# Optimization experiments

Measured on AMD Instinct MI355X. Metric: run time of the kernel, lower is better.

## Reference

```python
import jax, jax.numpy as jnp
import numpy as np

N_HEAD = 16
D_MODEL = 1024
D_K = D_MODEL // N_HEAD  # 64, also d_v
B, S = 8, 1024


def setup_inputs() -> dict:
    key = jax.random.key(0)
    ks = jax.random.split(key, 7)
    sc = 1.0 / np.sqrt(D_MODEL)
    return {
        "q": jax.random.normal(ks[0], (B, S, D_MODEL), jnp.float32),
        "k": jax.random.normal(ks[1], (B, S, D_MODEL), jnp.float32),
        "v": jax.random.normal(ks[2], (B, S, D_MODEL), jnp.float32),
        "Wq": jax.random.normal(ks[3], (N_HEAD, D_MODEL, D_K), jnp.float32) * sc,
        "Wk": jax.random.normal(ks[4], (N_HEAD, D_MODEL, D_K), jnp.float32) * sc,
        "Wv": jax.random.normal(ks[5], (D_MODEL, D_K), jnp.float32) * sc,  # shared across heads
        "Wo": jax.random.normal(ks[6], (D_K, D_MODEL), jnp.float32) * (1.0 / np.sqrt(D_K)),
    }


def reference(q, k, v, Wq, Wk, Wv, Wo):
    # Faithful to original: qs, ks, vs are ALL projected from q (k, v args unused),
    # and Wv is shared across all heads. Dropout is identity (rate 0 / eval).
    qs = jnp.einsum('bsd,hdk->hbsk', q, Wq)          # [H,B,S,dk]
    kk = jnp.einsum('bsd,hdk->hbsk', q, Wk)          # [H,B,S,dk]
    vs = jnp.einsum('bsd,dk->bsk', q, Wv)            # [B,S,dv] shared
    scale = 1.0 / jnp.sqrt(jnp.asarray(D_K, jnp.float32))
    scores = jnp.einsum('hbik,hbjk->hbij', qs, kk) * scale  # [H,B,S,S]
    attn = jax.nn.softmax(scores, axis=-1)
    head = jnp.einsum('hbij,bjk->hbik', attn, vs)    # [H,B,S,dv]
    pooled = jnp.mean(head, axis=0)                  # mean over heads, not concat
    out = jnp.einsum('bsk,kd->bsd', pooled, Wo)      # [B,S,d_model]
    return (out, attn)
```

## Files before the change

kernel.cpp:

```cpp
#include <hip/hip_runtime.h>
#include <hip/hip_bf16.h>
#include <stdint.h>

#define NC 2112

typedef __attribute__((ext_vector_type(8))) short bf16x8;
typedef __attribute__((ext_vector_type(4))) float f32x4;

static __device__ __forceinline__ unsigned short f2bf(float f) {
  uint32_t u = __builtin_bit_cast(uint32_t, f);
  u += 0x7FFFu + ((u >> 16) & 1u);
  return (unsigned short)(u >> 16);
}
static __device__ __forceinline__ unsigned short f2bf_n(float f) {
  __hip_bfloat16 h = __float2bfloat16(f);
  return __builtin_bit_cast(unsigned short, h);
}
static __device__ __forceinline__ float bf2f(unsigned short u) {
  return __builtin_bit_cast(float, ((uint32_t)u) << 16);
}
static __device__ __forceinline__ void gload16(const unsigned short* g, unsigned short* l) {
  __builtin_amdgcn_global_load_lds((const __attribute__((address_space(1))) void*)g,
                                   (__attribute__((address_space(3))) void*)l, 16, 0, 0);
}

__global__ void k_convert_q(const float* __restrict__ q, unsigned short* __restrict__ qbf) {
  int i = blockIdx.x * blockDim.x + threadIdx.x;
  float4 v = ((const float4*)q)[i];
  ushort4 o;
  o.x = f2bf(v.x); o.y = f2bf(v.y); o.z = f2bf(v.z); o.w = f2bf(v.w);
  ((ushort4*)qbf)[i] = o;
}

__global__ void k_build_wcatT(const float* __restrict__ Wq, const float* __restrict__ Wk,
                              const float* __restrict__ Wv, unsigned short* __restrict__ wt) {
  int t = blockIdx.x * blockDim.x + threadIdx.x;
  int c = t >> 7;
  int k0 = (t & 127) << 3;
  unsigned short o[8];
#pragma unroll
  for (int i = 0; i < 8; ++i) {
    int k = k0 + i;
    float v;
    if (c < 1024)      v = Wq[((size_t)(c >> 6) * 1024 + k) * 64 + (c & 63)];
    else if (c < 2048) v = Wk[((size_t)((c - 1024) >> 6) * 1024 + k) * 64 + (c & 63)];
    else               v = Wv[(size_t)k * 64 + (c - 2048)];
    o[i] = f2bf(v);
  }
  *(ushort4*)&wt[(size_t)c * 1024 + k0]     = *(ushort4*)&o[0];
  *(ushort4*)&wt[(size_t)c * 1024 + k0 + 4] = *(ushort4*)&o[4];
}

__global__ __launch_bounds__(256) void k_gemm(const unsigned short* __restrict__ A,
                                              const unsigned short* __restrict__ Bt,
                                              unsigned short* __restrict__ C,
                                              unsigned short* __restrict__ vst) {
  __shared__ unsigned short As[128 * 32];
  __shared__ unsigned short Bs[128 * 32];
  const int L = blockIdx.x;
  const int wi = (L & 7) * 136 + (L >> 3);
  const int tn = wi % 17, tm = wi / 17;
  const int rowBase = tm * 128, colBase = tn * 128;
  const int t = threadIdx.x;
  const int wave = t >> 6, lane = t & 63;
  const int wm = wave >> 1, wn = wave & 1;
  const int l15 = lane & 15, l4 = lane >> 4;
  f32x4 acc[4][4] = {};
  for (int kt = 0; kt < 1024; kt += 32) {
#pragma unroll
    for (int i = 0; i < 2; ++i) {
      int e = (t + i * 256) * 8;
      int r = e >> 5, c = e & 31;
      gload16(&A[(size_t)(rowBase + r) * 1024 + kt + c], &As[e]);
      int rb = colBase + r; rb = rb < NC ? rb : (NC - 1);
      gload16(&Bt[(size_t)rb * 1024 + kt + c], &Bs[e]);
    }
    __syncthreads();
    bf16x8 af[4], bfr[4];
#pragma unroll
    for (int m = 0; m < 4; ++m) af[m] = *(const bf16x8*)&As[(wm * 64 + m * 16 + l15) * 32 + l4 * 8];
#pragma unroll
    for (int n = 0; n < 4; ++n) bfr[n] = *(const bf16x8*)&Bs[(wn * 64 + n * 16 + l15) * 32 + l4 * 8];
#pragma unroll
    for (int m = 0; m < 4; ++m)
#pragma unroll
      for (int n = 0; n < 4; ++n)
        acc[m][n] = __builtin_amdgcn_mfma_f32_16x16x32_bf16(af[m], bfr[n], acc[m][n], 0, 0, 0);
    __syncthreads();
  }
#pragma unroll
  for (int m = 0; m < 4; ++m)
#pragma unroll
    for (int n = 0; n < 4; ++n) {
      int col = colBase + wn * 64 + n * 16 + l15;
      int row0 = rowBase + wm * 64 + m * 16 + l4 * 4;
      if (col < 2048) {
#pragma unroll
        for (int i = 0; i < 4; ++i)
          C[(size_t)(row0 + i) * NC + col] = f2bf_n(acc[m][n][i]);
      } else if (col < NC) {
        int d = col - 2048;
#pragma unroll
        for (int i = 0; i < 4; ++i) {
          int rg = row0 + i;
          vst[((size_t)(rg >> 10) * 64 + d) * 1024 + (rg & 1023)] = f2bf_n(acc[m][n][i]);
        }
      }
    }
}

__global__ __launch_bounds__(256, 4) void k_attn(const unsigned short* __restrict__ G,
                                                 const unsigned short* __restrict__ vst,
                                                 float* __restrict__ attn,
                                                 float* __restrict__ head) {
  __shared__ unsigned short SP[16][1032];
  __shared__ float rs[16][4];
  const int L = blockIdx.x;
  const int wi = (L & 7) * 1024 + (L >> 3);
  const int qt = wi & 63, b = (wi >> 6) & 7, h = wi >> 9;
  const int t = threadIdx.x, wave = t >> 6, lane = t & 63;
  const int l15 = lane & 15, l4 = lane >> 4;

  const unsigned short* Gb = G + (size_t)b * 1024 * NC;

  bf16x8 qf[2];
#pragma unroll
  for (int ks = 0; ks < 2; ++ks)
    qf[ks] = *(const bf16x8*)&Gb[(size_t)(qt * 16 + l15) * NC + h * 64 + ks * 32 + l4 * 8];

  const float scale = 0.125f;
  float psum[4] = {};
#pragma unroll
  for (int quarter = 0; quarter < 4; ++quarter) {
    bf16x8 kf[4][2];
#pragma unroll
    for (int kt = 0; kt < 4; ++kt) {
      int k0 = wave * 256 + quarter * 64 + kt * 16;
#pragma unroll
      for (int ks = 0; ks < 2; ++ks)
        kf[kt][ks] = *(const bf16x8*)&Gb[(size_t)(k0 + l15) * NC + 1024 + h * 64 + ks * 32 + l4 * 8];
    }
#pragma unroll
    for (int kt = 0; kt < 4; ++kt) {
      int k0 = wave * 256 + quarter * 64 + kt * 16;
      f32x4 s0 = {};
      s0 = __builtin_amdgcn_mfma_f32_16x16x32_bf16(qf[0], kf[kt][0], s0, 0, 0, 0);
      s0 = __builtin_amdgcn_mfma_f32_16x16x32_bf16(qf[1], kf[kt][1], s0, 0, 0, 0);
#pragma unroll
      for (int i = 0; i < 4; ++i) {
        unsigned short u = f2bf_n(__expf(s0[i] * scale));
        SP[l4 * 4 + i][k0 + l15] = u;
        psum[i] += bf2f(u);
      }
    }
  }
#pragma unroll
  for (int off = 1; off < 16; off <<= 1)
#pragma unroll
    for (int i = 0; i < 4; ++i)
      psum[i] += __shfl_xor(psum[i], off);
  if (l15 == 0) {
#pragma unroll
    for (int i = 0; i < 4; ++i)
      rs[l4 * 4 + i][wave] = psum[i];
  }
  __syncthreads();

  float winv[4], pinv[4];
#pragma unroll
  for (int rr = 0; rr < 4; ++rr) {
    float4 a = *(const float4*)&rs[wave * 4 + rr][0];
    winv[rr] = 1.0f / (a.x + a.y + a.z + a.w);
  }
#pragma unroll
  for (int i = 0; i < 4; ++i) {
    float4 a = *(const float4*)&rs[l4 * 4 + i][0];
    pinv[i] = 1.0f / (a.x + a.y + a.z + a.w);
  }

  size_t attn_base = ((size_t)(h * 8 + b) * 1024 + (size_t)qt * 16) * 1024;
#pragma unroll
  for (int rr = 0; rr < 4; ++rr) {
    int row = wave * 4 + rr;
    float inv = winv[rr];
#pragma unroll
    for (int c = 0; c < 2; ++c) {
      uint4 u = *(const uint4*)&SP[row][c * 512 + lane * 8];
      f32x4 p0 = {bf2f((unsigned short)(u.x & 0xFFFF)) * inv,
                  bf2f((unsigned short)(u.x >> 16)) * inv,
                  bf2f((unsigned short)(u.y & 0xFFFF)) * inv,
                  bf2f((unsigned short)(u.y >> 16)) * inv};
      f32x4 p1 = {bf2f((unsigned short)(u.z & 0xFFFF)) * inv,
                  bf2f((unsigned short)(u.z >> 16)) * inv,
                  bf2f((unsigned short)(u.w & 0xFFFF)) * inv,
                  bf2f((unsigned short)(u.w >> 16)) * inv};
      float* ab = &attn[attn_base + (size_t)row * 1024 + c * 512 + lane * 8];
      __builtin_nontemporal_store(p0, (f32x4*)ab);
      __builtin_nontemporal_store(p1, (f32x4*)(ab + 4));
    }
  }

  const unsigned short* vb = vst + ((size_t)b * 64 + wave * 16 + l15) * 1024;
  const unsigned short* pr = &SP[l15][0];
  f32x4 o0 = {}, o1 = {};
#pragma unroll 8
  for (int jt = 0; jt < 32; jt += 2) {
    bf16x8 pa0 = *(const bf16x8*)&pr[jt * 32 + l4 * 8];
    bf16x8 bv0 = *(const bf16x8*)&vb[jt * 32 + l4 * 8];
    o0 = __builtin_amdgcn_mfma_f32_16x16x32_bf16(pa0, bv0, o0, 0, 0, 0);
    bf16x8 pa1 = *(const bf16x8*)&pr[(jt + 1) * 32 + l4 * 8];
    bf16x8 bv1 = *(const bf16x8*)&vb[(jt + 1) * 32 + l4 * 8];
    o1 = __builtin_amdgcn_mfma_f32_16x16x32_bf16(pa1, bv1, o1, 0, 0, 0);
  }
  float* hb = head + (((size_t)(h * 8 + b) * 1024) + qt * 16) * 64 + wave * 16;
#pragma unroll
  for (int i = 0; i < 4; ++i)
    hb[(size_t)(l4 * 4 + i) * 64 + l15] = (o0[i] + o1[i]) * pinv[i];
}

__global__ __launch_bounds__(256) void k_final(const float* __restrict__ head,
                                               const float* __restrict__ Wo,
                                               float* __restrict__ out) {
  __shared__ float Ps[16][68];
  __shared__ float Ws[64][132];
  const int rt = blockIdx.x;
  const int r0 = rt * 16;
  const int t = threadIdx.x;
  {
    int r = t >> 4, k4 = (t & 15) * 4;
    float4 acc = {0.f, 0.f, 0.f, 0.f};
#pragma unroll
    for (int hh = 0; hh < 16; ++hh) {
      float4 v = *(const float4*)&head[((size_t)hh * 8192 + r0 + r) * 64 + k4];
      acc.x += v.x; acc.y += v.y; acc.z += v.z; acc.w += v.w;
    }
    const float s = 1.0f / 16.0f;
    Ps[r][k4] = acc.x * s; Ps[r][k4 + 1] = acc.y * s;
    Ps[r][k4 + 2] = acc.z * s; Ps[r][k4 + 3] = acc.w * s;
  }
  const int ty = t >> 4, tx = t & 15;
  for (int dt = 0; dt < 8; ++dt) {
    int d0 = dt * 128;
#pragma unroll
    for (int j = 0; j < 8; ++j) {
      int e = t + j * 256;
      int k = e >> 5, c4 = (e & 31) * 4;
      *(float4*)&Ws[k][c4] = *(const float4*)&Wo[(size_t)k * 1024 + d0 + c4];
    }
    __syncthreads();
    float acc[8] = {};
    for (int k = 0; k < 64; ++k) {
      float a0 = Ps[ty][k];
      float4 b0 = *(const float4*)&Ws[k][tx * 8];
      float4 b1 = *(const float4*)&Ws[k][tx * 8 + 4];
      acc[0] += a0 * b0.x; acc[1] += a0 * b0.y; acc[2] += a0 * b0.z; acc[3] += a0 * b0.w;
      acc[4] += a0 * b1.x; acc[5] += a0 * b1.y; acc[6] += a0 * b1.z; acc[7] += a0 * b1.w;
    }
    float4 v0 = {acc[0], acc[1], acc[2], acc[3]};
    float4 v1 = {acc[4], acc[5], acc[6], acc[7]};
    size_t o = (size_t)(r0 + ty) * 1024 + d0 + tx * 8;
    *(float4*)&out[o]     = v0;
    *(float4*)&out[o + 4] = v1;
    __syncthreads();
  }
}

extern "C" void kernel_launch(void* const* d_in, const int* in_sizes, int n_in,
                              void* d_out, int out_size, void* d_ws, size_t ws_size,
                              hipStream_t stream) {
  const float* q  = (const float*)d_in[0];
  const float* Wq = (const float*)d_in[3];
  const float* Wk = (const float*)d_in[4];
  const float* Wv = (const float*)d_in[5];
  const float* Wo = (const float*)d_in[6];

  char* ws = (char*)d_ws;
  unsigned short* qbf   = (unsigned short*)(ws + 0);
  unsigned short* wcatT = (unsigned short*)(ws + 16777216);
  unsigned short* G     = (unsigned short*)(ws + 21102592);
  unsigned short* vst   = (unsigned short*)(ws + 55705600);
  float*          head  = (float*)(ws + 56754176);

  float* out  = (float*)d_out;
  float* attn = out + (size_t)8 * 1024 * 1024;

  hipLaunchKernelGGL(k_convert_q,   dim3(8192), dim3(256), 0, stream, q, qbf);
  hipLaunchKernelGGL(k_build_wcatT, dim3(1056), dim3(256), 0, stream, Wq, Wk, Wv, wcatT);
  hipLaunchKernelGGL(k_gemm,        dim3(1088), dim3(256), 0, stream, qbf, wcatT, G, vst);
  hipLaunchKernelGGL(k_attn,        dim3(8192), dim3(256), 0, stream, G, vst, attn, head);
  hipLaunchKernelGGL(k_final,       dim3(512),  dim3(256), 0, stream, head, Wo, out);
}
```

Baseline: 401.5 us.

## Restructure attention into two-pass per-wave softmax with recomputed scores

Each wave now owns 16 query rows and sweeps all 1024 keys itself. A first pass computes only the row sums of exp(scores). A second pass recomputes QK^T, writes normalized probabilities straight to attn, and accumulates P·V in 64-key chunks through a small per-wave LDS tile. This removes the 16x1024 LDS buffer, the block-wide barrier and the cross-wave sum exchange, and cuts the grid from 8192 to 2048 blocks. The cost is doubling the QK^T MFMA work and K reads, and attn is now written with scattered 4-byte nontemporal stores instead of 16-byte vector stores.

```diff
diff --git a/kernel.cpp b/kernel.cpp
--- a/kernel.cpp
+++ b/kernel.cpp
@@ -113,109 +113,95 @@
                                                  const unsigned short* __restrict__ vst,
                                                  float* __restrict__ attn,
                                                  float* __restrict__ head) {
-  __shared__ unsigned short SP[16][1032];
-  __shared__ float rs[16][4];
+  __shared__ unsigned short SP[4][16][72];
   const int L = blockIdx.x;
-  const int wi = (L & 7) * 1024 + (L >> 3);
-  const int qt = wi & 63, b = (wi >> 6) & 7, h = wi >> 9;
+  const int wi = (L & 7) * 256 + (L >> 3);
+  const int qt = wi & 15, b = (wi >> 4) & 7, h = wi >> 7;
   const int t = threadIdx.x, wave = t >> 6, lane = t & 63;
   const int l15 = lane & 15, l4 = lane >> 4;
+  const int qrow0 = qt * 64 + wave * 16;
+  const float scale = 0.125f;
 
   const unsigned short* Gb = G + (size_t)b * 1024 * NC;
-
-  bf16x8 qf[2];
-#pragma unroll
-  for (int ks = 0; ks < 2; ++ks)
-    qf[ks] = *(const bf16x8*)&Gb[(size_t)(qt * 16 + l15) * NC + h * 64 + ks * 32 + l4 * 8];
-
-  const float scale = 0.125f;
+  const unsigned short* Kb = Gb + 1024 + h * 64 + l4 * 8;
+  const unsigned short* Qp = Gb + (size_t)(qrow0 + l15) * NC + h * 64 + l4 * 8;
+  bf16x8 qf0 = *(const bf16x8*)Qp;
+  bf16x8 qf1 = *(const bf16x8*)(Qp + 32);
+
   float psum[4] = {};
-#pragma unroll
-  for (int quarter = 0; quarter < 4; ++quarter) {
+#pragma unroll 2
+  for (int seg = 0; seg < 16; ++seg) {
     bf16x8 kf[4][2];
 #pragma unroll
     for (int kt = 0; kt < 4; ++kt) {
-      int k0 = wave * 256 + quarter * 64 + kt * 16;
-#pragma unroll
-      for (int ks = 0; ks < 2; ++ks)
-        kf[kt][ks] = *(const bf16x8*)&Gb[(size_t)(k0 + l15) * NC + 1024 + h * 64 + ks * 32 + l4 * 8];
+      const unsigned short* kp = Kb + (size_t)(seg * 64 + kt * 16 + l15) * NC;
+      kf[kt][0] = *(const bf16x8*)kp;
+      kf[kt][1] = *(const bf16x8*)(kp + 32);
     }
 #pragma unroll
     for (int kt = 0; kt < 4; ++kt) {
-      int k0 = wave * 256 + quarter * 64 + kt * 16;
-      f32x4 s0 = {};
-      s0 = __builtin_amdgcn_mfma_f32_16x16x32_bf16(qf[0], kf[kt][0], s0, 0, 0, 0);
-      s0 = __builtin_amdgcn_mfma_f32_16x16x32_bf16(qf[1], kf[kt][1], s0, 0, 0, 0);
-#pragma unroll
-      for (int i = 0; i < 4; ++i) {
-        unsigned short u = f2bf_n(__expf(s0[i] * scale));
-        SP[l4 * 4 + i][k0 + l15] = u;
-        psum[i] += bf2f(u);
+      f32x4 s = {};
+      s = __builtin_amdgcn_mfma_f32_16x16x32_bf16(qf0, kf[kt][0], s, 0, 0, 0);
+      s = __builtin_amdgcn_mfma_f32_16x16x32_bf16(qf1, kf[kt][1], s, 0, 0, 0);
+#pragma unroll
+      for (int i = 0; i < 4; ++i) psum[i] += __expf(s[i] * scale);
+    }
+  }
+#pragma unroll
+  for (int off = 1; off < 16; off <<= 1)
+#pragma unroll
+    for (int i = 0; i < 4; ++i) psum[i] += __shfl_xor(psum[i], off);
+  float inv[4];
+#pragma unroll
+  for (int i = 0; i < 4; ++i) inv[i] = 1.0f / psum[i];
+
+  size_t abase = ((size_t)(h * 8 + b) * 1024 + qrow0) * 1024;
+  const unsigned short* Vb = vst + (size_t)b * 65536 + (size_t)l15 * 1024 + l4 * 8;
+  f32x4 oacc[4] = {};
+#pragma unroll 2
+  for (int seg = 0; seg < 16; ++seg) {
+#pragma unroll
+    for (int ht = 0; ht < 2; ++ht) {
+      bf16x8 kf[2][2];
+#pragma unroll
+      for (int ktl = 0; ktl < 2; ++ktl) {
+        const unsigned short* kp = Kb + (size_t)(seg * 64 + (ht * 2 + ktl) * 16 + l15) * NC;
+        kf[ktl][0] = *(const bf16x8*)kp;
+        kf[ktl][1] = *(const bf16x8*)(kp + 32);
       }
-    }
-  }
-#pragma unroll
-  for (int off = 1; off < 16; off <<= 1)
+#pragma unroll
+      for (int ktl = 0; ktl < 2; ++ktl) {
+        int kt = ht * 2 + ktl;
+        f32x4 s = {};
+        s = __builtin_amdgcn_mfma_f32_16x16x32_bf16(qf0, kf[ktl][0], s, 0, 0, 0);
+        s = __builtin_amdgcn_mfma_f32_16x16x32_bf16(qf1, kf[ktl][1], s, 0, 0, 0);
+        int key = seg * 64 + kt * 16 + l15;
+#pragma unroll
+        for (int i = 0; i < 4; ++i) {
+          float e = __expf(s[i] * scale);
+          __builtin_nontemporal_store(e * inv[i],
+              &attn[abase + (size_t)(l4 * 4 + i) * 1024 + key]);
+          SP[wave][l4 * 4 + i][kt * 16 + l15] = f2bf_n(e);
+        }
+      }
+    }
+    bf16x8 pa0 = *(const bf16x8*)&SP[wave][l15][l4 * 8];
+    bf16x8 pa1 = *(const bf16x8*)&SP[wave][l15][32 + l4 * 8];
+#pragma unroll
+    for (int n = 0; n < 4; ++n) {
+      const unsigned short* vp = Vb + (size_t)n * 16384 + seg * 64;
+      bf16x8 v0 = *(const bf16x8*)vp;
+      bf16x8 v1 = *(const bf16x8*)(vp + 32);
+      oacc[n] = __builtin_amdgcn_mfma_f32_16x16x32_bf16(pa0, v0, oacc[n], 0, 0, 0);
+      oacc[n] = __builtin_amdgcn_mfma_f32_16x16x32_bf16(pa1, v1, oacc[n], 0, 0, 0);
+    }
+  }
+  float* hb = head + ((size_t)(h * 8 + b) * 1024 + qrow0) * 64;
+#pragma unroll
+  for (int n = 0; n < 4; ++n)
 #pragma unroll
     for (int i = 0; i < 4; ++i)
-      psum[i] += __shfl_xor(psum[i], off);
-  if (l15 == 0) {
-#pragma unroll
-    for (int i = 0; i < 4; ++i)
-      rs[l4 * 4 + i][wave] = psum[i];
-  }
-  __syncthreads();
-
-  float winv[4], pinv[4];
-#pragma unroll
-  for (int rr = 0; rr < 4; ++rr) {
-    float4 a = *(const float4*)&rs[wave * 4 + rr][0];
-    winv[rr] = 1.0f / (a.x + a.y + a.z + a.w);
-  }
-#pragma unroll
-  for (int i = 0; i < 4; ++i) {
-    float4 a = *(const float4*)&rs[l4 * 4 + i][0];
-    pinv[i] = 1.0f / (a.x + a.y + a.z + a.w);
-  }
-
-  size_t attn_base = ((size_t)(h * 8 + b) * 1024 + (size_t)qt * 16) * 1024;
-#pragma unroll
-  for (int rr = 0; rr < 4; ++rr) {
-    int row = wave * 4 + rr;
-    float inv = winv[rr];
-#pragma unroll
-    for (int c = 0; c < 2; ++c) {
-      uint4 u = *(const uint4*)&SP[row][c * 512 + lane * 8];
-      f32x4 p0 = {bf2f((unsigned short)(u.x & 0xFFFF)) * inv,
-                  bf2f((unsigned short)(u.x >> 16)) * inv,
-                  bf2f((unsigned short)(u.y & 0xFFFF)) * inv,
-                  bf2f((unsigned short)(u.y >> 16)) * inv};
-      f32x4 p1 = {bf2f((unsigned short)(u.z & 0xFFFF)) * inv,
-                  bf2f((unsigned short)(u.z >> 16)) * inv,
-                  bf2f((unsigned short)(u.w & 0xFFFF)) * inv,
-                  bf2f((unsigned short)(u.w >> 16)) * inv};
-      float* ab = &attn[attn_base + (size_t)row * 1024 + c * 512 + lane * 8];
-      __builtin_nontemporal_store(p0, (f32x4*)ab);
-      __builtin_nontemporal_store(p1, (f32x4*)(ab + 4));
-    }
-  }
-
-  const unsigned short* vb = vst + ((size_t)b * 64 + wave * 16 + l15) * 1024;
-  const unsigned short* pr = &SP[l15][0];
-  f32x4 o0 = {}, o1 = {};
-#pragma unroll 8
-  for (int jt = 0; jt < 32; jt += 2) {
-    bf16x8 pa0 = *(const bf16x8*)&pr[jt * 32 + l4 * 8];
-    bf16x8 bv0 = *(const bf16x8*)&vb[jt * 32 + l4 * 8];
-    o0 = __builtin_amdgcn_mfma_f32_16x16x32_bf16(pa0, bv0, o0, 0, 0, 0);
-    bf16x8 pa1 = *(const bf16x8*)&pr[(jt + 1) * 32 + l4 * 8];
-    bf16x8 bv1 = *(const bf16x8*)&vb[(jt + 1) * 32 + l4 * 8];
-    o1 = __builtin_amdgcn_mfma_f32_16x16x32_bf16(pa1, bv1, o1, 0, 0, 0);
-  }
-  float* hb = head + (((size_t)(h * 8 + b) * 1024) + qt * 16) * 64 + wave * 16;
-#pragma unroll
-  for (int i = 0; i < 4; ++i)
-    hb[(size_t)(l4 * 4 + i) * 64 + l15] = (o0[i] + o1[i]) * pinv[i];
+      hb[(size_t)(l4 * 4 + i) * 64 + n * 16 + l15] = oacc[n][i] * inv[i];
 }
 
 __global__ __launch_bounds__(256) void k_final(const float* __restrict__ head,
@@ -287,6 +273,6 @@
   hipLaunchKernelGGL(k_convert_q,   dim3(8192), dim3(256), 0, stream, q, qbf);
   hipLaunchKernelGGL(k_build_wcatT, dim3(1056), dim3(256), 0, stream, Wq, Wk, Wv, wcatT);
   hipLaunchKernelGGL(k_gemm,        dim3(1088), dim3(256), 0, stream, qbf, wcatT, G, vst);
-  hipLaunchKernelGGL(k_attn,        dim3(8192), dim3(256), 0, stream, G, vst, attn, head);
+  hipLaunchKernelGGL(k_attn,        dim3(2048), dim3(256), 0, stream, G, vst, attn, head);
   hipLaunchKernelGGL(k_final,       dim3(512),  dim3(256), 0, stream, head, Wo, out);
 }
```

Result: slower. 477.7 us (+19.0%).

## Double attention query tile to 32 rows with 8-wave blocks and vectorized P stores

Applied to the files above, without the earlier changes.

The attention kernel now handles 32 query rows per block using 512 threads (8 waves), so each loaded K fragment is reused for two query sub-tiles. QK^T is computed with K as the A operand, which lets each lane write four consecutive bf16 probabilities as one 64-bit LDS store, and row sums are reduced with two shuffles instead of four. The PV MFMA and head store now run before the attn store, and the launch is halved to 4096 blocks. The cost is doubled LDS per block (about 66KB), which may lower occupancy, and higher register pressure under the 512-thread launch bound.

```diff
diff --git a/kernel.cpp b/kernel.cpp
--- a/kernel.cpp
+++ b/kernel.cpp
@@ -109,76 +109,103 @@
     }
 }
 
-__global__ __launch_bounds__(256, 4) void k_attn(const unsigned short* __restrict__ G,
+__global__ __launch_bounds__(512, 4) void k_attn(const unsigned short* __restrict__ G,
                                                  const unsigned short* __restrict__ vst,
                                                  float* __restrict__ attn,
                                                  float* __restrict__ head) {
-  __shared__ unsigned short SP[16][1032];
-  __shared__ float rs[16][4];
+  __shared__ unsigned short SP[32][1032];
+  __shared__ float rs[32][8];
   const int L = blockIdx.x;
-  const int wi = (L & 7) * 1024 + (L >> 3);
-  const int qt = wi & 63, b = (wi >> 6) & 7, h = wi >> 9;
+  const int wi = (L & 7) * 512 + (L >> 3);
+  const int qt = wi & 31, b = (wi >> 5) & 7, h = wi >> 8;
   const int t = threadIdx.x, wave = t >> 6, lane = t & 63;
   const int l15 = lane & 15, l4 = lane >> 4;
+  const float scale = 0.125f;
 
   const unsigned short* Gb = G + (size_t)b * 1024 * NC;
 
-  bf16x8 qf[2];
-#pragma unroll
-  for (int ks = 0; ks < 2; ++ks)
-    qf[ks] = *(const bf16x8*)&Gb[(size_t)(qt * 16 + l15) * NC + h * 64 + ks * 32 + l4 * 8];
-
-  const float scale = 0.125f;
-  float psum[4] = {};
-#pragma unroll
-  for (int quarter = 0; quarter < 4; ++quarter) {
+  bf16x8 qf[2][2];
+#pragma unroll
+  for (int m = 0; m < 2; ++m)
+#pragma unroll
+    for (int ks = 0; ks < 2; ++ks)
+      qf[m][ks] = *(const bf16x8*)&Gb[(size_t)(qt * 32 + m * 16 + l15) * NC + h * 64 + ks * 32 + l4 * 8];
+
+  float psum[2] = {};
+#pragma unroll
+  for (int half = 0; half < 2; ++half) {
     bf16x8 kf[4][2];
 #pragma unroll
     for (int kt = 0; kt < 4; ++kt) {
-      int k0 = wave * 256 + quarter * 64 + kt * 16;
+      int k0 = wave * 128 + half * 64 + kt * 16;
 #pragma unroll
       for (int ks = 0; ks < 2; ++ks)
         kf[kt][ks] = *(const bf16x8*)&Gb[(size_t)(k0 + l15) * NC + 1024 + h * 64 + ks * 32 + l4 * 8];
     }
 #pragma unroll
     for (int kt = 0; kt < 4; ++kt) {
-      int k0 = wave * 256 + quarter * 64 + kt * 16;
-      f32x4 s0 = {};
-      s0 = __builtin_amdgcn_mfma_f32_16x16x32_bf16(qf[0], kf[kt][0], s0, 0, 0, 0);
-      s0 = __builtin_amdgcn_mfma_f32_16x16x32_bf16(qf[1], kf[kt][1], s0, 0, 0, 0);
-#pragma unroll
-      for (int i = 0; i < 4; ++i) {
-        unsigned short u = f2bf_n(__expf(s0[i] * scale));
-        SP[l4 * 4 + i][k0 + l15] = u;
-        psum[i] += bf2f(u);
+      int k0 = wave * 128 + half * 64 + kt * 16;
+#pragma unroll
+      for (int m = 0; m < 2; ++m) {
+        f32x4 s = {};
+        s = __builtin_amdgcn_mfma_f32_16x16x32_bf16(kf[kt][0], qf[m][0], s, 0, 0, 0);
+        s = __builtin_amdgcn_mfma_f32_16x16x32_bf16(kf[kt][1], qf[m][1], s, 0, 0, 0);
+        float e0 = __expf(s[0] * scale), e1 = __expf(s[1] * scale);
+        float e2 = __expf(s[2] * scale), e3 = __expf(s[3] * scale);
+        psum[m] += (e0 + e1) + (e2 + e3);
+        uint32_t lo = (uint32_t)f2bf_n(e0) | ((uint32_t)f2bf_n(e1) << 16);
+        uint32_t hi = (uint32_t)f2bf_n(e2) | ((uint32_t)f2bf_n(e3) << 16);
+        uint2 u = {lo, hi};
+        *(uint2*)&SP[m * 16 + l15][k0 + l4 * 4] = u;
       }
     }
   }
 #pragma unroll
-  for (int off = 1; off < 16; off <<= 1)
-#pragma unroll
-    for (int i = 0; i < 4; ++i)
-      psum[i] += __shfl_xor(psum[i], off);
-  if (l15 == 0) {
-#pragma unroll
-    for (int i = 0; i < 4; ++i)
-      rs[l4 * 4 + i][wave] = psum[i];
+  for (int m = 0; m < 2; ++m) {
+    psum[m] += __shfl_xor(psum[m], 16);
+    psum[m] += __shfl_xor(psum[m], 32);
+  }
+  if (l4 == 0) {
+    rs[l15][wave]      = psum[0];
+    rs[16 + l15][wave] = psum[1];
   }
   __syncthreads();
 
+  const int wm = wave >> 2, wn = wave & 3;
   float winv[4], pinv[4];
 #pragma unroll
   for (int rr = 0; rr < 4; ++rr) {
-    float4 a = *(const float4*)&rs[wave * 4 + rr][0];
-    winv[rr] = 1.0f / (a.x + a.y + a.z + a.w);
+    int row = wave * 4 + rr;
+    float4 a = *(const float4*)&rs[row][0];
+    float4 c = *(const float4*)&rs[row][4];
+    winv[rr] = 1.0f / (a.x + a.y + a.z + a.w + c.x + c.y + c.z + c.w);
   }
 #pragma unroll
   for (int i = 0; i < 4; ++i) {
-    float4 a = *(const float4*)&rs[l4 * 4 + i][0];
-    pinv[i] = 1.0f / (a.x + a.y + a.z + a.w);
-  }
-
-  size_t attn_base = ((size_t)(h * 8 + b) * 1024 + (size_t)qt * 16) * 1024;
+    int row = wm * 16 + l4 * 4 + i;
+    float4 a = *(const float4*)&rs[row][0];
+    float4 c = *(const float4*)&rs[row][4];
+    pinv[i] = 1.0f / (a.x + a.y + a.z + a.w + c.x + c.y + c.z + c.w);
+  }
+
+  const unsigned short* vb = vst + ((size_t)b * 64 + wn * 16 + l15) * 1024;
+  const unsigned short* pr = &SP[wm * 16 + l15][0];
+  f32x4 o0 = {}, o1 = {};
+#pragma unroll 8
+  for (int jt = 0; jt < 32; jt += 2) {
+    bf16x8 pa0 = *(const bf16x8*)&pr[jt * 32 + l4 * 8];
+    bf16x8 bv0 = *(const bf16x8*)&vb[jt * 32 + l4 * 8];
+    o0 = __builtin_amdgcn_mfma_f32_16x16x32_bf16(pa0, bv0, o0, 0, 0, 0);
+    bf16x8 pa1 = *(const bf16x8*)&pr[(jt + 1) * 32 + l4 * 8];
+    bf16x8 bv1 = *(const bf16x8*)&vb[(jt + 1) * 32 + l4 * 8];
+    o1 = __builtin_amdgcn_mfma_f32_16x16x32_bf16(pa1, bv1, o1, 0, 0, 0);
+  }
+  float* hb = head + (((size_t)(h * 8 + b) * 1024) + qt * 32 + wm * 16) * 64 + wn * 16;
+#pragma unroll
+  for (int i = 0; i < 4; ++i)
+    hb[(size_t)(l4 * 4 + i) * 64 + l15] = (o0[i] + o1[i]) * pinv[i];
+
+  size_t attn_base = ((size_t)(h * 8 + b) * 1024 + (size_t)qt * 32) * 1024;
 #pragma unroll
   for (int rr = 0; rr < 4; ++rr) {
     int row = wave * 4 + rr;
@@ -199,23 +226,6 @@
       __builtin_nontemporal_store(p1, (f32x4*)(ab + 4));
     }
   }
-
-  const unsigned short* vb = vst + ((size_t)b * 64 + wave * 16 + l15) * 1024;
-  const unsigned short* pr = &SP[l15][0];
-  f32x4 o0 = {}, o1 = {};
-#pragma unroll 8
-  for (int jt = 0; jt < 32; jt += 2) {
-    bf16x8 pa0 = *(const bf16x8*)&pr[jt * 32 + l4 * 8];
-    bf16x8 bv0 = *(const bf16x8*)&vb[jt * 32 + l4 * 8];
-    o0 = __builtin_amdgcn_mfma_f32_16x16x32_bf16(pa0, bv0, o0, 0, 0, 0);
-    bf16x8 pa1 = *(const bf16x8*)&pr[(jt + 1) * 32 + l4 * 8];
-    bf16x8 bv1 = *(const bf16x8*)&vb[(jt + 1) * 32 + l4 * 8];
-    o1 = __builtin_amdgcn_mfma_f32_16x16x32_bf16(pa1, bv1, o1, 0, 0, 0);
-  }
-  float* hb = head + (((size_t)(h * 8 + b) * 1024) + qt * 16) * 64 + wave * 16;
-#pragma unroll
-  for (int i = 0; i < 4; ++i)
-    hb[(size_t)(l4 * 4 + i) * 64 + l15] = (o0[i] + o1[i]) * pinv[i];
 }
 
 __global__ __launch_bounds__(256) void k_final(const float* __restrict__ head,
@@ -287,6 +297,6 @@
   hipLaunchKernelGGL(k_convert_q,   dim3(8192), dim3(256), 0, stream, q, qbf);
   hipLaunchKernelGGL(k_build_wcatT, dim3(1056), dim3(256), 0, stream, Wq, Wk, Wv, wcatT);
   hipLaunchKernelGGL(k_gemm,        dim3(1088), dim3(256), 0, stream, qbf, wcatT, G, vst);
-  hipLaunchKernelGGL(k_attn,        dim3(8192), dim3(256), 0, stream, G, vst, attn, head);
+  hipLaunchKernelGGL(k_attn,        dim3(4096), dim3(512), 0, stream, G, vst, attn, head);
   hipLaunchKernelGGL(k_final,       dim3(512),  dim3(256), 0, stream, head, Wo, out);
 }
```

Result: faster. 379.0 us (-5.6%).
